# Kernel tuning notes

Measured on AMD Instinct MI355X. Metric: run time of the kernel, lower is better.

## Reference

```python
import jax, jax.numpy as jnp
import numpy as np

B, S, H, N, D = 2, 2048, 1024, 16, 64  # batch, seq, hidden, heads, head_size
PAD = -30000.0


def setup_inputs() -> dict:
    key = jax.random.key(0)
    kx, kqkv, kout, krpe = jax.random.split(key, 4)
    x = jax.random.normal(kx, (B, S, H), jnp.float32)
    qkv = jax.random.normal(kqkv, (H, 3, N, D), jnp.float32) * H ** (-0.5)
    out_w = jax.random.normal(kout, (N, D, H), jnp.float32) * (N * D) ** (-0.5)
    # rpe_bias is zero-init in torch; use small randn so the bias path is exercised
    rpe_bias = jax.random.normal(krpe, (N, S), jnp.float32) * 0.02
    return {"x": x, "qkv": qkv, "out_w": out_w, "rpe_bias": rpe_bias}


def reference(x, qkv, out_w, rpe_bias):
    # q, k, v: [B, N, S, D]
    q, k, v = jnp.einsum('bsx,xMnd->Mbnsd', x, qkv)
    s = x.shape[1]
    a = jnp.einsum('bnsd,bntd->bnst', q, k) * q.shape[-1] ** (-0.5)
    # cumulative relative-position bias: bias[n, i, j] = cumsum(rpe)[n, i-j] for i>=j,
    # PAD otherwise (exactly what to_tril produces on the row-broadcast cumsum).
    cum = jnp.cumsum(rpe_bias[:, :s], axis=-1)            # [N, S]
    rel = jnp.arange(s)[:, None] - jnp.arange(s)[None, :]  # [S, S], i - j
    bias = jnp.where(rel >= 0, cum[:, jnp.clip(rel, 0)], PAD)  # [N, S, S]
    a = jax.nn.softmax(a + bias, axis=-1)
    mix = jnp.einsum('bnst,bntd->bnsd', a, v)
    return jnp.einsum('bnsd,ndx->bsx', mix, out_w)
```

## Files before the change

kernel.cpp:

```cpp
#include <hip/hip_runtime.h>
#include <hip/hip_bf16.h>
#include <cstdint>
#include <cstddef>

#define B_   2
#define S_   2048
#define H_   1024
#define NH   16
#define DH   64
#define LOG2E 1.4426950408889634f
#define SCALE2 (0.125f * LOG2E)

typedef __hip_bfloat16 bf16;
typedef short bf16x8 __attribute__((ext_vector_type(8)));
typedef float f32x4 __attribute__((ext_vector_type(4)));

#define MFMA16(a, b, c) __builtin_amdgcn_mfma_f32_16x16x32_bf16((a), (b), (c), 0, 0, 0)

__device__ __forceinline__ void async16(const void* g, void* l) {
  __builtin_amdgcn_global_load_lds(
      (const __attribute__((address_space(1))) void*)g,
      (__attribute__((address_space(3))) void*)l,
      16, 0, 0);
}

__device__ __forceinline__ void tr_body(const float* __restrict__ src,
                                        bf16* __restrict__ dst, int R, int C,
                                        int c0, int r0, bf16 (*tile)[33], int tid) {
  int tx = tid & 31, ty = tid >> 5;
  for (int i = 0; i < 32; i += 8)
    tile[ty + i][tx] = __float2bfloat16(src[(size_t)(r0 + ty + i) * C + c0 + tx]);
  __syncthreads();
  for (int i = 0; i < 32; i += 8)
    dst[(size_t)(c0 + ty + i) * R + r0 + tx] = tile[tx][ty + i];
}

__global__ __launch_bounds__(256)
void prep(const float* __restrict__ x, bf16* __restrict__ xb,
          const float* __restrict__ qkv, bf16* __restrict__ qkvT,
          const float* __restrict__ outw, bf16* __restrict__ outwT,
          const float* __restrict__ rpe, float* __restrict__ cum) {
  __shared__ char pm[2176] __attribute__((aligned(16)));
  const int L = blockIdx.x, tid = threadIdx.x;
  if (L < 4096) {
    int i = (L * 256 + tid) * 4;
    float4 v = *(const float4*)(x + i);
    bf16 o[4] = {__float2bfloat16(v.x), __float2bfloat16(v.y),
                 __float2bfloat16(v.z), __float2bfloat16(v.w)};
    *(uint64_t*)(xb + i) = *(const uint64_t*)o;
  } else if (L < 7168) {
    int t = L - 4096;
    int cx = t % 96, ry = t / 96;
    tr_body(qkv, qkvT, 1024, 3072, cx * 32, ry * 32, (bf16(*)[33])pm, tid);
  } else if (L < 8192) {
    int t = L - 7168;
    int cx = t & 31, ry = t >> 5;
    tr_body(outw, outwT, 1024, 1024, cx * 32, ry * 32, (bf16(*)[33])pm, tid);
  } else {
    float* ssum = (float*)pm;
    int n = L - 8192;
    float loc[8];
    float s = 0.f;
    int base = tid * 8;
#pragma unroll
    for (int u = 0; u < 8; ++u) {
      loc[u] = rpe[n * S_ + base + u];
      s += loc[u];
    }
    ssum[tid] = s;
    __syncthreads();
    float own = s;
    for (int off = 1; off < 256; off <<= 1) {
      float v = (tid >= off) ? ssum[tid - off] : 0.f;
      __syncthreads();
      ssum[tid] += v;
      __syncthreads();
    }
    float run = ssum[tid] - own;
#pragma unroll
    for (int u = 0; u < 8; ++u) {
      run += loc[u];
      cum[n * S_ + base + u] = run * LOG2E;
    }
  }
}

template <int MODE>
__global__ __launch_bounds__(256, MODE == 0 ? 3 : 2)
void gemm_bt(const bf16* __restrict__ A, const bf16* __restrict__ Bt,
             bf16* __restrict__ C0, bf16* __restrict__ C1, bf16* __restrict__ C2,
             float* __restrict__ F0) {
  constexpr int NT = (MODE == 0) ? 4 : 2;
  constexpr int NB = NT * 32;
  __shared__ char smem[MODE == 0 ? 36864 : 12288] __attribute__((aligned(16)));
  bf16* As = (bf16*)smem;
  bf16* Bs = (bf16*)(smem + 8192);
  const int tid = threadIdx.x, lane = tid & 63, w = tid >> 6;
  const int lr = lane & 15, lq = lane >> 4;
  const int m0 = blockIdx.y * 128, n0 = blockIdx.x * NB;
  const int wm = (w & 1) * 64, wn = (w >> 1) * (NT * 16);

  f32x4 acc[4][NT] = {};

  for (int k0 = 0; k0 < 1024; k0 += 32) {
    __syncthreads();
#pragma unroll
    for (int t = 0; t < 2; ++t) {
      int c = (t * 4 + w) * 64 + lane;
      int row = c >> 2, ch = c & 3;
      int k8 = (ch ^ ((row >> 1) & 3)) * 8;
      async16(A + (size_t)(m0 + row) * 1024 + k0 + k8,
              (char*)As + (size_t)(t * 4 + w) * 1024 + lane * 16);
    }
#pragma unroll
    for (int t = 0; t < NB / 64; ++t) {
      int c = (t * 4 + w) * 64 + lane;
      int row = c >> 2, ch = c & 3;
      int k8 = (ch ^ ((row >> 1) & 3)) * 8;
      async16(Bt + (size_t)(n0 + row) * 1024 + k0 + k8,
              (char*)Bs + (size_t)(t * 4 + w) * 1024 + lane * 16);
    }
    __syncthreads();
    bf16x8 af[4], bfr[NT];
#pragma unroll
    for (int mt = 0; mt < 4; ++mt) {
      int row = wm + mt * 16 + lr;
      af[mt] = *(const bf16x8*)(As + row * 32 + ((lq ^ ((row >> 1) & 3)) << 3));
    }
#pragma unroll
    for (int nt = 0; nt < NT; ++nt) {
      int row = wn + nt * 16 + lr;
      bfr[nt] = *(const bf16x8*)(Bs + row * 32 + ((lq ^ ((row >> 1) & 3)) << 3));
    }
#pragma unroll
    for (int mt = 0; mt < 4; ++mt)
#pragma unroll
      for (int nt = 0; nt < NT; ++nt)
        acc[mt][nt] = MFMA16(af[mt], bfr[nt], acc[mt][nt]);
  }

  if (MODE == 0) {
    __syncthreads();
    bf16* E = (bf16*)smem + w * (64 * 72);
    const int cbase = n0 + wn;
    const int mm = cbase >> 10, nn = (cbase >> 6) & 15;
    const int bb = (m0 + wm) >> 11;
    const int sbase = (m0 + wm) & 2047;
    if (mm < 2) {
#pragma unroll
      for (int mt = 0; mt < 4; ++mt)
#pragma unroll
        for (int nt = 0; nt < 4; ++nt)
#pragma unroll
          for (int r = 0; r < 4; ++r)
            E[(mt * 16 + lq * 4 + r) * 72 + nt * 16 + lr] =
                __float2bfloat16(acc[mt][nt][r]);
      bf16* dst = (mm == 0 ? C0 : C1) +
                  ((size_t)(bb * NH + nn) * S_ + sbase) * DH;
#pragma unroll
      for (int it = 0; it < 8; ++it) {
        int c = it * 64 + lane;
        int rw = c >> 3, c8 = c & 7;
        *(uint4*)(dst + (size_t)rw * DH + c8 * 8) =
            *(const uint4*)(E + rw * 72 + c8 * 8);
      }
    } else {
#pragma unroll
      for (int mt = 0; mt < 4; ++mt)
#pragma unroll
        for (int nt = 0; nt < 4; ++nt)
#pragma unroll
          for (int r = 0; r < 4; ++r)
            E[(nt * 16 + lr) * 72 + mt * 16 + lq * 4 + r] =
                __float2bfloat16(acc[mt][nt][r]);
      bf16* dst = C2 + (size_t)(bb * NH + nn) * DH * S_;
#pragma unroll
      for (int it = 0; it < 8; ++it) {
        int c = it * 64 + lane;
        int dr = c >> 3, c8 = c & 7;
        *(uint4*)(dst + (size_t)dr * S_ + sbase + c8 * 8) =
            *(const uint4*)(E + dr * 72 + c8 * 8);
      }
    }
  } else {
#pragma unroll
    for (int mt = 0; mt < 4; ++mt)
#pragma unroll
      for (int nt = 0; nt < NT; ++nt)
#pragma unroll
        for (int r = 0; r < 4; ++r) {
          int rM = m0 + wm + mt * 16 + lq * 4 + r;
          int cN = n0 + wn + nt * 16 + lr;
          F0[(size_t)rM * 1024 + cN] = acc[mt][nt][r];
        }
  }
}

__global__ __launch_bounds__(256, 2)
void fa_kernel(const bf16* __restrict__ q, const bf16* __restrict__ k,
               const bf16* __restrict__ vt, const float* __restrict__ cum,
               bf16* __restrict__ mix) {
  __shared__ char smem[53248] __attribute__((aligned(16)));
  bf16* Ps = (bf16*)(smem + 32768);
  float* cumS = (float*)(smem + 50176);

  const int tid = threadIdx.x, lane = tid & 63, w = tid >> 6;
  const int lr = lane & 15, lq = lane >> 4;

  const int L = blockIdx.x;
  const int xcd = L & 7, slot = L >> 3;
  const int bn = xcd + 8 * (slot & 3);
  const int pr = slot >> 2;
  const int n = bn & (NH - 1);
  const int b = bn >> 4;
  const float* cumn = cum + n * S_;

  bf16x8 ones;
#pragma unroll
  for (int u = 0; u < 8; ++u) ones[u] = (short)0x3F80;

  const int iloc = w * 16 + lr;

  for (int ph = 0; ph < 2; ++ph) {
    const int ti = ph ? pr : (31 - pr);
    const int i0 = ti * 64;
    const int nj = (ti >> 1) + 1;

    const bf16* qbase = q + ((size_t)bn * S_ + i0 + w * 16) * DH;
    bf16x8 qf[2];
#pragma unroll
    for (int kt = 0; kt < 2; ++kt)
      qf[kt] = *(const bf16x8*)(qbase + lr * DH + kt * 32 + lq * 8);

    f32x4 oacc[4] = {};
    f32x4 lacc = {};

    for (int jt = 0; jt < nj; ++jt) {
      const int j0 = jt * 128;
      const bool diag = (jt == nj - 1);
      __syncthreads();

      const char* ksrc = (const char*)(k + ((size_t)bn * S_ + j0) * DH);
#pragma unroll
      for (int t = 0; t < 4; ++t) {
        int cb = t * 4 + w;
        int row = cb * 8 + (lane >> 3);
        int cs = (lane & 7) ^ (row & 7);
        async16(ksrc + row * 128 + cs * 16, smem + cb * 1024 + lane * 16);
      }
      const char* vsrc = (const char*)(vt + (size_t)bn * DH * S_);
#pragma unroll
      for (int t = 0; t < 4; ++t) {
        int cb = t * 4 + w;
        int row = cb * 4 + (lane >> 4);
        int cs = (lane & 15) ^ (row & 15);
        async16(vsrc + (size_t)row * (S_ * 2) + j0 * 2 + cs * 16,
                smem + 16384 + cb * 1024 + lane * 16);
      }
      if (tid < 192) {
        int base = i0 - j0 - 127 + tid;
#pragma unroll
        for (int p = 0; p < 4; ++p) {
          int src = base + p;
          src = src < 0 ? 0 : (src > S_ - 1 ? S_ - 1 : src);
          cumS[p * 192 + tid] = cumn[src];
        }
      }
      __syncthreads();

      f32x4 sa[8] = {};
#pragma unroll
      for (int kt = 0; kt < 2; ++kt)
#pragma unroll
        for (int nt = 0; nt < 8; ++nt) {
          int krow = nt * 16 + lr;
          bf16x8 kf = *(const bf16x8*)(smem + krow * 128 +
                          (((kt * 4 + lq) ^ (krow & 7)) << 4));
          sa[nt] = MFMA16(kf, qf[kt], sa[nt]);
        }

      const int doff = i0 - j0;
      if (!diag) {
#pragma unroll
        for (int nt = 0; nt < 8; ++nt) {
          int jl = nt * 16 + lq * 4;
          int Xm3 = 124 + iloc - jl;
          int p = Xm3 & 3, b0 = Xm3 & ~3;
          f32x4 cv = *(const f32x4*)(cumS + p * 192 + b0);
          bf16 pk[4];
#pragma unroll
          for (int r = 0; r < 4; ++r)
            pk[r] = __float2bfloat16(exp2f(sa[nt][r] * SCALE2 + cv[3 - r]));
          *(uint64_t*)(Ps + iloc * 136 + nt * 16 + lq * 4) = *(const uint64_t*)pk;
        }
      } else {
#pragma unroll
        for (int nt = 0; nt < 8; ++nt) {
          int jl = nt * 16 + lq * 4;
          int Xm3 = 124 + iloc - jl;
          int p = Xm3 & 3, b0 = Xm3 & ~3;
          f32x4 cv = *(const f32x4*)(cumS + p * 192 + b0);
          bf16 pk[4];
#pragma unroll
          for (int r = 0; r < 4; ++r) {
            float pv = (doff + iloc - jl - r >= 0)
                           ? exp2f(sa[nt][r] * SCALE2 + cv[3 - r])
                           : 0.f;
            pk[r] = __float2bfloat16(pv);
          }
          *(uint64_t*)(Ps + iloc * 136 + nt * 16 + lq * 4) = *(const uint64_t*)pk;
        }
      }

#pragma unroll
      for (int kt2 = 0; kt2 < 4; ++kt2) {
        bf16x8 pf = *(const bf16x8*)(Ps + (w * 16 + lr) * 136 + kt2 * 32 + lq * 8);
        lacc = MFMA16(pf, ones, lacc);
#pragma unroll
        for (int dt = 0; dt < 4; ++dt) {
          int vrow = dt * 16 + lr;
          bf16x8 vf = *(const bf16x8*)(smem + 16384 + vrow * 256 +
                          (((kt2 * 4 + lq) ^ (vrow & 15)) << 4));
          oacc[dt] = MFMA16(pf, vf, oacc[dt]);
        }
      }
    }

#pragma unroll
    for (int dt = 0; dt < 4; ++dt)
#pragma unroll
      for (int r = 0; r < 4; ++r) {
        int i = i0 + w * 16 + lq * 4 + r;
        int d = dt * 16 + lr;
        mix[((size_t)(b * S_ + i) * NH + n) * DH + d] =
            __float2bfloat16(oacc[dt][r] / lacc[r]);
      }
  }
}

extern "C" void kernel_launch(void* const* d_in, const int* in_sizes, int n_in,
                              void* d_out, int out_size, void* d_ws, size_t ws_size,
                              hipStream_t stream) {
  const float* x     = (const float*)d_in[0];
  const float* qkv   = (const float*)d_in[1];
  const float* out_w = (const float*)d_in[2];
  const float* rpe   = (const float*)d_in[3];
  float* out = (float*)d_out;

  char* ws = (char*)d_ws;
  bf16* qkvT  = (bf16*)(ws + 0);
  bf16* outwT = (bf16*)(ws + 6291456);
  bf16* xb    = (bf16*)(ws + 8388608);
  bf16* qb    = (bf16*)(ws + 16777216);
  bf16* kb    = (bf16*)(ws + 25165824);
  bf16* vtb   = (bf16*)(ws + 33554432);
  bf16* mixb  = (bf16*)(ws + 41943040);
  float* cum  = (float*)(ws + 50331648);

  prep<<<8208, 256, 0, stream>>>(x, xb, qkv, qkvT, out_w, outwT, rpe, cum);
  gemm_bt<0><<<dim3(3072 / 128, 4096 / 128), 256, 0, stream>>>(xb, qkvT, qb, kb, vtb, nullptr);
  fa_kernel<<<512, 256, 0, stream>>>(qb, kb, vtb, cum, mixb);
  gemm_bt<1><<<dim3(1024 / 64, 4096 / 128), 256, 0, stream>>>(mixb, outwT, nullptr, nullptr, nullptr, out);
}
```

Before: 179.9 us.

## Double-buffer K/V/bias tiles and widen FA query tile to 128 rows

Restructures the attention kernel so each workgroup processes 128 query rows (two 16-row sub-tiles per wave), halving the grid to 256 blocks. K, V and cumulative-bias tiles are double-buffered in LDS and prefetched asynchronously (bias now via 4-byte global_load_lds) while the current tile is computed, removing one barrier per iteration. The two causal tile pairs are flattened into a single 17-step loop. This trades occupancy (one block per CU, ~106KB LDS, more registers) and a smaller grid for more K/V reuse and overlap of loads with compute.

```diff
diff --git a/kernel.cpp b/kernel.cpp
--- a/kernel.cpp
+++ b/kernel.cpp
@@ -22,6 +22,12 @@
       (const __attribute__((address_space(1))) void*)g,
       (__attribute__((address_space(3))) void*)l,
       16, 0, 0);
+}
+__device__ __forceinline__ void async4(const void* g, void* l) {
+  __builtin_amdgcn_global_load_lds(
+      (const __attribute__((address_space(1))) void*)g,
+      (__attribute__((address_space(3))) void*)l,
+      4, 0, 0);
 }
 
 __device__ __forceinline__ void tr_body(const float* __restrict__ src,
@@ -196,13 +202,45 @@
   }
 }
 
-__global__ __launch_bounds__(256, 2)
+__device__ __forceinline__ void fa_stage(const bf16* __restrict__ k,
+                                         const bf16* __restrict__ vt,
+                                         const float* __restrict__ cumn,
+                                         char* smem, int bn, int i0p, int j0p,
+                                         int buf, int lane, int w, int tid) {
+  char* dst = smem + buf * 32768;
+  const char* ksrc = (const char*)(k + ((size_t)bn * S_ + j0p) * DH);
+#pragma unroll
+  for (int t = 0; t < 4; ++t) {
+    int cb = t * 4 + w;
+    int row = cb * 8 + (lane >> 3);
+    int cs = (lane & 7) ^ (row & 7);
+    async16(ksrc + row * 128 + cs * 16, dst + cb * 1024 + lane * 16);
+  }
+  const char* vsrc = (const char*)(vt + (size_t)bn * DH * S_);
+#pragma unroll
+  for (int t = 0; t < 4; ++t) {
+    int cb = t * 4 + w;
+    int row = cb * 4 + (lane >> 4);
+    int cs = (lane & 15) ^ (row & 15);
+    async16(vsrc + (size_t)row * (S_ * 2) + j0p * 2 + cs * 16,
+            dst + 16384 + cb * 1024 + lane * 16);
+  }
+  float* cdst = (float*)(smem + 100352) + buf * 1056;
+  int base = i0p - j0p - 127 + tid;
+#pragma unroll
+  for (int p = 0; p < 4; ++p) {
+    int src = base + p;
+    src = src < 0 ? 0 : (src > S_ - 1 ? S_ - 1 : src);
+    async4(cumn + src, cdst + p * 264 + w * 64 + lane);
+  }
+}
+
+__global__ __launch_bounds__(256, 1)
 void fa_kernel(const bf16* __restrict__ q, const bf16* __restrict__ k,
                const bf16* __restrict__ vt, const float* __restrict__ cum,
                bf16* __restrict__ mix) {
-  __shared__ char smem[53248] __attribute__((aligned(16)));
-  bf16* Ps = (bf16*)(smem + 32768);
-  float* cumS = (float*)(smem + 50176);
+  __shared__ char smem[108800] __attribute__((aligned(16)));
+  bf16* Ps = (bf16*)(smem + 65536);
 
   const int tid = threadIdx.x, lane = tid & 63, w = tid >> 6;
   const int lr = lane & 15, lq = lane >> 4;
@@ -215,126 +253,133 @@
   const int b = bn >> 4;
   const float* cumn = cum + n * S_;
 
+  const int T0 = 15 - pr;
+  const int T1 = pr;
+  const int nj0 = T0 + 1;
+
   bf16x8 ones;
 #pragma unroll
   for (int u = 0; u < 8; ++u) ones[u] = (short)0x3F80;
-
-  const int iloc = w * 16 + lr;
-
-  for (int ph = 0; ph < 2; ++ph) {
-    const int ti = ph ? pr : (31 - pr);
-    const int i0 = ti * 64;
-    const int nj = (ti >> 1) + 1;
-
-    const bf16* qbase = q + ((size_t)bn * S_ + i0 + w * 16) * DH;
-    bf16x8 qf[2];
+  const f32x4 fz = {0.f, 0.f, 0.f, 0.f};
+
+  fa_stage(k, vt, cumn, smem, bn, T0 << 7, 0, 0, lane, w, tid);
+
+  f32x4 oacc[2][4];
+  f32x4 lacc[2];
+  bf16x8 qf[2][2];
+  int ti = T0, jt = 0, i0 = T0 << 7;
+
+  for (int g = 0; g < 17; ++g) {
+    const int bsel = g & 1;
+    const char* kb = smem + bsel * 32768;
+    const char* vb = kb + 16384;
+    const float* cumB = (const float*)(smem + 100352) + bsel * 1056;
+    const bool diag = (jt == ti);
+
+    __syncthreads();
+
+    if (g + 1 < 17) {
+      int gn = g + 1, tin, jtn;
+      if (gn < nj0) { tin = T0; jtn = gn; }
+      else          { tin = T1; jtn = gn - nj0; }
+      fa_stage(k, vt, cumn, smem, bn, tin << 7, jtn << 7, bsel ^ 1, lane, w, tid);
+    }
+
+    if (jt == 0) {
+      const bf16* qbase = q + ((size_t)bn * S_ + i0 + w * 32) * DH;
+#pragma unroll
+      for (int is = 0; is < 2; ++is)
+#pragma unroll
+        for (int kt = 0; kt < 2; ++kt)
+          qf[is][kt] = *(const bf16x8*)(qbase + (is * 16 + lr) * DH + kt * 32 + lq * 8);
+#pragma unroll
+      for (int is = 0; is < 2; ++is) {
+        lacc[is] = fz;
+#pragma unroll
+        for (int dt = 0; dt < 4; ++dt) oacc[is][dt] = fz;
+      }
+    }
+
+    f32x4 sa[2][8] = {};
 #pragma unroll
     for (int kt = 0; kt < 2; ++kt)
-      qf[kt] = *(const bf16x8*)(qbase + lr * DH + kt * 32 + lq * 8);
-
-    f32x4 oacc[4] = {};
-    f32x4 lacc = {};
-
-    for (int jt = 0; jt < nj; ++jt) {
-      const int j0 = jt * 128;
-      const bool diag = (jt == nj - 1);
-      __syncthreads();
-
-      const char* ksrc = (const char*)(k + ((size_t)bn * S_ + j0) * DH);
-#pragma unroll
-      for (int t = 0; t < 4; ++t) {
-        int cb = t * 4 + w;
-        int row = cb * 8 + (lane >> 3);
-        int cs = (lane & 7) ^ (row & 7);
-        async16(ksrc + row * 128 + cs * 16, smem + cb * 1024 + lane * 16);
-      }
-      const char* vsrc = (const char*)(vt + (size_t)bn * DH * S_);
-#pragma unroll
-      for (int t = 0; t < 4; ++t) {
-        int cb = t * 4 + w;
-        int row = cb * 4 + (lane >> 4);
-        int cs = (lane & 15) ^ (row & 15);
-        async16(vsrc + (size_t)row * (S_ * 2) + j0 * 2 + cs * 16,
-                smem + 16384 + cb * 1024 + lane * 16);
-      }
-      if (tid < 192) {
-        int base = i0 - j0 - 127 + tid;
-#pragma unroll
-        for (int p = 0; p < 4; ++p) {
-          int src = base + p;
-          src = src < 0 ? 0 : (src > S_ - 1 ? S_ - 1 : src);
-          cumS[p * 192 + tid] = cumn[src];
-        }
-      }
-      __syncthreads();
-
-      f32x4 sa[8] = {};
-#pragma unroll
-      for (int kt = 0; kt < 2; ++kt)
-#pragma unroll
-        for (int nt = 0; nt < 8; ++nt) {
-          int krow = nt * 16 + lr;
-          bf16x8 kf = *(const bf16x8*)(smem + krow * 128 +
-                          (((kt * 4 + lq) ^ (krow & 7)) << 4));
-          sa[nt] = MFMA16(kf, qf[kt], sa[nt]);
-        }
-
-      const int doff = i0 - j0;
+#pragma unroll
+      for (int nt = 0; nt < 8; ++nt) {
+        int krow = nt * 16 + lr;
+        bf16x8 kf = *(const bf16x8*)(kb + krow * 128 +
+                        (((kt * 4 + lq) ^ (krow & 7)) << 4));
+        sa[0][nt] = MFMA16(kf, qf[0][kt], sa[0][nt]);
+        sa[1][nt] = MFMA16(kf, qf[1][kt], sa[1][nt]);
+      }
+
+#pragma unroll
+    for (int is = 0; is < 2; ++is) {
+      const int ilocI = w * 32 + is * 16 + lr;
       if (!diag) {
 #pragma unroll
         for (int nt = 0; nt < 8; ++nt) {
           int jl = nt * 16 + lq * 4;
-          int Xm3 = 124 + iloc - jl;
+          int Xm3 = 124 + ilocI - jl;
           int p = Xm3 & 3, b0 = Xm3 & ~3;
-          f32x4 cv = *(const f32x4*)(cumS + p * 192 + b0);
+          f32x4 cv = *(const f32x4*)(cumB + p * 264 + b0);
           bf16 pk[4];
 #pragma unroll
           for (int r = 0; r < 4; ++r)
-            pk[r] = __float2bfloat16(exp2f(sa[nt][r] * SCALE2 + cv[3 - r]));
-          *(uint64_t*)(Ps + iloc * 136 + nt * 16 + lq * 4) = *(const uint64_t*)pk;
+            pk[r] = __float2bfloat16(exp2f(sa[is][nt][r] * SCALE2 + cv[3 - r]));
+          *(uint64_t*)(Ps + ilocI * 136 + nt * 16 + lq * 4) = *(const uint64_t*)pk;
         }
       } else {
 #pragma unroll
         for (int nt = 0; nt < 8; ++nt) {
           int jl = nt * 16 + lq * 4;
-          int Xm3 = 124 + iloc - jl;
+          int Xm3 = 124 + ilocI - jl;
           int p = Xm3 & 3, b0 = Xm3 & ~3;
-          f32x4 cv = *(const f32x4*)(cumS + p * 192 + b0);
+          f32x4 cv = *(const f32x4*)(cumB + p * 264 + b0);
           bf16 pk[4];
 #pragma unroll
           for (int r = 0; r < 4; ++r) {
-            float pv = (doff + iloc - jl - r >= 0)
-                           ? exp2f(sa[nt][r] * SCALE2 + cv[3 - r])
+            float pv = (ilocI - jl - r >= 0)
+                           ? exp2f(sa[is][nt][r] * SCALE2 + cv[3 - r])
                            : 0.f;
             pk[r] = __float2bfloat16(pv);
           }
-          *(uint64_t*)(Ps + iloc * 136 + nt * 16 + lq * 4) = *(const uint64_t*)pk;
+          *(uint64_t*)(Ps + ilocI * 136 + nt * 16 + lq * 4) = *(const uint64_t*)pk;
         }
       }
-
-#pragma unroll
-      for (int kt2 = 0; kt2 < 4; ++kt2) {
-        bf16x8 pf = *(const bf16x8*)(Ps + (w * 16 + lr) * 136 + kt2 * 32 + lq * 8);
-        lacc = MFMA16(pf, ones, lacc);
-#pragma unroll
-        for (int dt = 0; dt < 4; ++dt) {
-          int vrow = dt * 16 + lr;
-          bf16x8 vf = *(const bf16x8*)(smem + 16384 + vrow * 256 +
-                          (((kt2 * 4 + lq) ^ (vrow & 15)) << 4));
-          oacc[dt] = MFMA16(pf, vf, oacc[dt]);
-        }
-      }
-    }
-
-#pragma unroll
-    for (int dt = 0; dt < 4; ++dt)
-#pragma unroll
-      for (int r = 0; r < 4; ++r) {
-        int i = i0 + w * 16 + lq * 4 + r;
-        int d = dt * 16 + lr;
-        mix[((size_t)(b * S_ + i) * NH + n) * DH + d] =
-            __float2bfloat16(oacc[dt][r] / lacc[r]);
-      }
+    }
+
+#pragma unroll
+    for (int kt2 = 0; kt2 < 4; ++kt2) {
+      bf16x8 pf0 = *(const bf16x8*)(Ps + (w * 32 + lr) * 136 + kt2 * 32 + lq * 8);
+      bf16x8 pf1 = *(const bf16x8*)(Ps + (w * 32 + 16 + lr) * 136 + kt2 * 32 + lq * 8);
+      lacc[0] = MFMA16(pf0, ones, lacc[0]);
+      lacc[1] = MFMA16(pf1, ones, lacc[1]);
+#pragma unroll
+      for (int dt = 0; dt < 4; ++dt) {
+        int vrow = dt * 16 + lr;
+        bf16x8 vf = *(const bf16x8*)(vb + vrow * 256 +
+                        (((kt2 * 4 + lq) ^ (vrow & 15)) << 4));
+        oacc[0][dt] = MFMA16(pf0, vf, oacc[0][dt]);
+        oacc[1][dt] = MFMA16(pf1, vf, oacc[1][dt]);
+      }
+    }
+
+    if (diag) {
+#pragma unroll
+      for (int is = 0; is < 2; ++is)
+#pragma unroll
+        for (int dt = 0; dt < 4; ++dt)
+#pragma unroll
+          for (int r = 0; r < 4; ++r) {
+            int i = i0 + w * 32 + is * 16 + lq * 4 + r;
+            int d = dt * 16 + lr;
+            mix[((size_t)(b * S_ + i) * NH + n) * DH + d] =
+                __float2bfloat16(oacc[is][dt][r] / lacc[is][r]);
+          }
+      ti = T1; jt = 0; i0 = T1 << 7;
+    } else {
+      ++jt;
+    }
   }
 }
 
@@ -359,6 +404,6 @@
 
   prep<<<8208, 256, 0, stream>>>(x, xb, qkv, qkvT, out_w, outwT, rpe, cum);
   gemm_bt<0><<<dim3(3072 / 128, 4096 / 128), 256, 0, stream>>>(xb, qkvT, qb, kb, vtb, nullptr);
-  fa_kernel<<<512, 256, 0, stream>>>(qb, kb, vtb, cum, mixb);
+  fa_kernel<<<256, 256, 0, stream>>>(qb, kb, vtb, cum, mixb);
   gemm_bt<1><<<dim3(1024 / 64, 4096 / 128), 256, 0, stream>>>(mixb, outwT, nullptr, nullptr, nullptr, out);
 }
```

Result: slower. 205.6 us (+14.3%).
